# Kernel optimization log

Measured on AMD Instinct MI355X. Metric: run time of the kernel, lower is better.

Reference implementation:

```python
import jax, jax.numpy as jnp
import numpy as np

N_NODES = 100000
N_EDGES = 1600000
EDGES_IN = 1
HID = 64
OUT = 64


def setup_inputs() -> dict:
    key = jax.random.key(0)
    ks = jax.random.split(key, 10)
    s = lambda fan_in: 1.0 / np.sqrt(fan_in)
    inp = {
        "edge_index": jax.random.randint(ks[0], (2, N_EDGES), 0, N_NODES, dtype=jnp.int64) if jax.config.jax_enable_x64 else jax.random.randint(ks[0], (2, N_EDGES), 0, N_NODES, dtype=jnp.int32),
        "edge_attr": jax.random.normal(ks[1], (N_EDGES, EDGES_IN), dtype=jnp.float32),
        # edge MLP: Linear(EDGES_IN->HID), SiLU, Linear(HID->HID), SiLU
        "W1": jax.random.uniform(ks[2], (EDGES_IN, HID), jnp.float32, -s(EDGES_IN), s(EDGES_IN)),
        "b1": jax.random.uniform(ks[3], (HID,), jnp.float32, -s(EDGES_IN), s(EDGES_IN)),
        "W2": jax.random.uniform(ks[4], (HID, HID), jnp.float32, -s(HID), s(HID)),
        "b2": jax.random.uniform(ks[5], (HID,), jnp.float32, -s(HID), s(HID)),
        # node MLP: Linear(HID->HID), SiLU, Linear(HID->OUT)
        "W3": jax.random.uniform(ks[6], (HID, HID), jnp.float32, -s(HID), s(HID)),
        "b3": jax.random.uniform(ks[7], (HID,), jnp.float32, -s(HID), s(HID)),
        "W4": jax.random.uniform(ks[8], (HID, OUT), jnp.float32, -s(HID), s(HID)),
        "b4": jax.random.uniform(ks[9], (OUT,), jnp.float32, -s(HID), s(HID)),
    }
    return inp


def reference(edge_index, edge_attr, W1, b1, W2, b2, W3, b3, W4, b4):
    silu = jax.nn.silu
    # edge model: [E, EDGES_IN] -> [E, HID]
    ef = silu(edge_attr @ W1 + b1)
    ef = silu(ef @ W2 + b2)
    # unsorted_segment_sum over source nodes (row): [E, HID] -> [N, HID]
    row = edge_index[0]
    agg = jax.ops.segment_sum(ef, row, num_segments=N_NODES)
    # node model: [N, HID] -> [N, OUT]
    h = silu(agg @ W3 + b3) @ W4 + b4
    return h
```

## Files before the change

### kernel.cpp

```cpp
#include <hip/hip_runtime.h>
#include <math.h>
#include <utility>

#define TN 4096
#define XMIN (-8.0f)
#define XMAX (8.0f)

#define GB1 256
#define MAXBK 2048
#define BKN 64
#define BKCAP 1792

typedef __attribute__((ext_vector_type(8))) short short8;
typedef __attribute__((ext_vector_type(4))) float f32x4;

__device__ __forceinline__ float silu_f(float v) {
    return v / (1.0f + __expf(-v));
}

__device__ __forceinline__ unsigned short f2bf(float x) {
    unsigned u = __float_as_uint(x);
    return (unsigned short)((u + 0x7FFFu + ((u >> 16) & 1u)) >> 16);
}
__device__ __forceinline__ float bf2f(unsigned short h) {
    return __uint_as_float(((unsigned)h) << 16);
}

#define SPLIT8(w0,w1,w2,w3,w4,w5,w6,w7, H, L) { \
    unsigned short _h0=f2bf(w0),_h1=f2bf(w1),_h2=f2bf(w2),_h3=f2bf(w3), \
                   _h4=f2bf(w4),_h5=f2bf(w5),_h6=f2bf(w6),_h7=f2bf(w7); \
    H = (short8){(short)_h0,(short)_h1,(short)_h2,(short)_h3, \
                 (short)_h4,(short)_h5,(short)_h6,(short)_h7}; \
    L = (short8){(short)f2bf((w0)-bf2f(_h0)),(short)f2bf((w1)-bf2f(_h1)), \
                 (short)f2bf((w2)-bf2f(_h2)),(short)f2bf((w3)-bf2f(_h3)), \
                 (short)f2bf((w4)-bf2f(_h4)),(short)f2bf((w5)-bf2f(_h5)), \
                 (short)f2bf((w6)-bf2f(_h6)),(short)f2bf((w7)-bf2f(_h7))}; }

#define BFRAG(Wp, kc, nt, H, L) { \
    const float* _p = (Wp) + ((kc)*32 + quad*8)*64 + (nt)*16 + m; \
    SPLIT8(_p[0],_p[64],_p[128],_p[192],_p[256],_p[320],_p[384],_p[448], H, L) }

#define MFMA3(AH, AL, BH, BL, ACC) \
    ACC = __builtin_amdgcn_mfma_f32_16x16x32_bf16(AH, BH, ACC, 0, 0, 0); \
    ACC = __builtin_amdgcn_mfma_f32_16x16x32_bf16(AL, BH, ACC, 0, 0, 0); \
    ACC = __builtin_amdgcn_mfma_f32_16x16x32_bf16(AH, BL, ACC, 0, 0, 0);

__global__ void build_table_k(const float* __restrict__ W1, const float* __restrict__ b1,
                              const float* __restrict__ W2, const float* __restrict__ b2,
                              float* __restrict__ table2, int* __restrict__ cnt, int nbk) {
    int gid  = blockIdx.x * blockDim.x + threadIdx.x;
    if (gid < nbk) cnt[gid] = 0;
    int wave = gid >> 6;
    int lane = gid & 63;
    if (wave >= TN) return;
    const float step = (XMAX - XMIN) / (float)(TN - 1);
    float x  = XMIN + step * (float)wave;
    float h1 = silu_f(fmaf(x, W1[lane], b1[lane]));
    float acc = b2[lane];
#pragma unroll
    for (int k = 0; k < 64; ++k) {
        float h1k = __shfl(h1, k, 64);
        acc = fmaf(h1k, W2[k * 64 + lane], acc);
    }
    float val = silu_f(acc);
    table2[(size_t)wave * 128 + 2 * lane] = val;
    if (wave > 0)
        table2[(size_t)(wave - 1) * 128 + 2 * lane + 1] = val;
}

__global__ void pack_w_k(const float* __restrict__ W3, const float* __restrict__ W4,
                         short8* __restrict__ packW) {
    int t = threadIdx.x, lane = t & 63, wid = t >> 6;
    int m = lane & 15, quad = lane >> 4;
    for (int f = wid; f < 16; f += 4) {
        const float* Wp = (f < 8) ? W3 : W4;
        int kc = f & 1, nt = (f >> 1) & 3;
        short8 H, L;
        BFRAG(Wp, kc, nt, H, L)
        packW[(2 * f + 0) * 64 + lane] = H;
        packW[(2 * f + 1) * 64 + lane] = L;
    }
}

__global__ void bhist_k(const int* __restrict__ row, int* __restrict__ cnt,
                        int E, int nbk) {
    __shared__ int h[MAXBK];
    int t = threadIdx.x;
    for (int e = t; e < nbk; e += 256) h[e] = 0;
    __syncthreads();
    for (int i = blockIdx.x * 256 + t; i < E; i += 256 * GB1)
        atomicAdd(&h[row[i] >> 6], 1);
    __syncthreads();
    for (int e = t; e < nbk; e += 256)
        if (h[e]) atomicAdd(&cnt[e], h[e]);
}

__global__ void scan1_k(const int* __restrict__ cnt, int* __restrict__ bhs,
                        int* __restrict__ cur, int n) {
    __shared__ int b0[MAXBK], b1[MAXBK];
    int t = threadIdx.x;
    for (int e = t; e < MAXBK; e += 1024) b0[e] = (e < n) ? cnt[e] : 0;
    __syncthreads();
    int* src = b0; int* dst = b1;
    for (int d = 1; d < MAXBK; d <<= 1) {
        for (int e = t; e < MAXBK; e += 1024)
            dst[e] = src[e] + ((e >= d) ? src[e - d] : 0);
        __syncthreads();
        int* tmp = src; src = dst; dst = tmp;
    }
    for (int e = t; e < n; e += 1024) {
        int v = (e == 0) ? 0 : src[e - 1];
        bhs[e] = v; cur[e] = v;
    }
    if (t == 0) bhs[n] = src[n - 1];
}

__global__ void bscatter_k(const int* __restrict__ row, const float* __restrict__ x,
                           int* __restrict__ cur, unsigned int* __restrict__ packed,
                           int E, int nbk) {
    __shared__ int hist[MAXBK];
    int t = threadIdx.x;
    for (int e = t; e < nbk; e += 256) hist[e] = 0;
    __syncthreads();
    for (int i = blockIdx.x * 256 + t; i < E; i += 256 * GB1)
        atomicAdd(&hist[row[i] >> 6], 1);
    __syncthreads();
    int shift = (int)(((long)blockIdx.x * nbk) >> 8);
    for (int k = t; k < nbk; k += 256) {
        int e = k + shift; if (e >= nbk) e -= nbk;
        int c = hist[e];
        hist[e] = c ? atomicAdd(&cur[e], c) : 0;
    }
    __syncthreads();
    const float scale = (float)(TN - 1) / (XMAX - XMIN);
    for (int i = blockIdx.x * 256 + t; i < E; i += 256 * GB1) {
        int   r  = row[i];
        float xv = x[i];
        float tt = fminf(fmaxf((xv - XMIN) * scale, 0.f), (float)(TN - 1) - 0.001f);
        int   i0 = (int)tt;
        unsigned int q = min((unsigned int)((tt - (float)i0) * 8192.0f), 8191u);
        unsigned int pk = ((unsigned int)(r & 63) << 25) | ((unsigned int)i0 << 13) | q;
        int p = atomicAdd(&hist[r >> 6], 1);
        packed[p] = pk;
    }
}

__global__ __launch_bounds__(256, 8)
void gather_k(const unsigned int* __restrict__ packed, const int* __restrict__ bhs,
              const float* __restrict__ table2, float* __restrict__ aggOut, int N) {
    __shared__ unsigned int srt[BKCAP];
    __shared__ int hist[BKN + 1];
    __shared__ int curs[BKN];
    int t = threadIdx.x, lane = t & 63, wid = t >> 6;
    int b = blockIdx.x;

    int s   = bhs[b];
    int e_  = bhs[b + 1];
    int cnt = min(e_ - s, BKCAP);

    for (int i = t; i <= BKN; i += 256) hist[i] = 0;
    __syncthreads();
    for (int i = t; i < cnt; i += 256)
        atomicAdd(&hist[packed[s + i] >> 25], 1);
    __syncthreads();

    if (wid == 0) {
        int c = hist[lane];
        int sc = c;
#pragma unroll
        for (int d = 1; d < 64; d <<= 1) {
            int u = __shfl_up(sc, d, 64);
            if (lane >= d) sc += u;
        }
        hist[lane] = sc - c;  curs[lane] = sc - c;
        if (lane == 63) hist[BKN] = sc;
    }
    __syncthreads();

    for (int i = t; i < cnt; i += 256) {
        unsigned int p = packed[s + i];
        int pos = atomicAdd(&curs[p >> 25], 1);
        srt[pos] = p;
    }
    __syncthreads();

    const float2* tab = (const float2*)table2 + lane;
    for (int nl = wid; nl < BKN; nl += 4) {
        int n = (b << 6) + nl;
        if (n >= N) break;
        int beg = hist[nl], dn = hist[nl + 1] - beg;
        float a0 = 0.f, a1 = 0.f, a2 = 0.f, a3 = 0.f;
        int j = 0;
        for (; j + 4 <= dn; j += 4) {
            unsigned int p0 = srt[beg + j + 0];
            unsigned int p1 = srt[beg + j + 1];
            unsigned int p2 = srt[beg + j + 2];
            unsigned int p3 = srt[beg + j + 3];
            float2 uv0 = tab[(p0 >> 7) & 0x3FFC0u];
            float2 uv1 = tab[(p1 >> 7) & 0x3FFC0u];
            float2 uv2 = tab[(p2 >> 7) & 0x3FFC0u];
            float2 uv3 = tab[(p3 >> 7) & 0x3FFC0u];
            float f0 = (float)(p0 & 0x1FFFu) * (1.0f / 8192.0f);
            float f1 = (float)(p1 & 0x1FFFu) * (1.0f / 8192.0f);
            float f2 = (float)(p2 & 0x1FFFu) * (1.0f / 8192.0f);
            float f3 = (float)(p3 & 0x1FFFu) * (1.0f / 8192.0f);
            a0 = fmaf(f0, uv0.y - uv0.x, a0 + uv0.x);
            a1 = fmaf(f1, uv1.y - uv1.x, a1 + uv1.x);
            a2 = fmaf(f2, uv2.y - uv2.x, a2 + uv2.x);
            a3 = fmaf(f3, uv3.y - uv3.x, a3 + uv3.x);
        }
        for (; j < dn; ++j) {
            unsigned int p0 = srt[beg + j];
            float2 uv0 = tab[(p0 >> 7) & 0x3FFC0u];
            float f0 = (float)(p0 & 0x1FFFu) * (1.0f / 8192.0f);
            a0 = fmaf(f0, uv0.y - uv0.x, a0 + uv0.x);
        }
        aggOut[(size_t)n * 64 + lane] = (a0 + a1) + (a2 + a3);
    }
}

__global__ __launch_bounds__(256, 1)
void mlp_k(const short8* __restrict__ packW, const float* __restrict__ b3,
           const float* __restrict__ b4, float* __restrict__ h, int N) {
    __shared__ float gt[4][16 * 68];
    int t = threadIdx.x, lane = t & 63, wid = t >> 6;
    int m = lane & 15, quad = lane >> 4;
    long r0 = (long)blockIdx.x * 64 + wid * 16;
    if (r0 >= N) return;

    const short8* pw = packW + lane;
#define LDW(s) pw[(s) * 64]
    short8 B3h00=LDW( 0), B3l00=LDW( 1), B3h01=LDW( 2), B3l01=LDW( 3);
    short8 B3h10=LDW( 4), B3l10=LDW( 5), B3h11=LDW( 6), B3l11=LDW( 7);
    short8 B3h20=LDW( 8), B3l20=LDW( 9), B3h21=LDW(10), B3l21=LDW(11);
    short8 B3h30=LDW(12), B3l30=LDW(13), B3h31=LDW(14), B3l31=LDW(15);
    short8 B4h00=LDW(16), B4l00=LDW(17), B4h01=LDW(18), B4l01=LDW(19);
    short8 B4h10=LDW(20), B4l10=LDW(21), B4h11=LDW(22), B4l11=LDW(23);
    short8 B4h20=LDW(24), B4l20=LDW(25), B4h21=LDW(26), B4l21=LDW(27);
    short8 B4h30=LDW(28), B4l30=LDW(29), B4h31=LDW(30), B4l31=LDW(31);
#undef LDW

    long ra = r0 + m; if (ra > N - 1) ra = N - 1;
    const float* ap = h + ra * 64 + quad * 8;
    float4 p0 = *(const float4*)(ap);       float4 p1 = *(const float4*)(ap + 4);
    float4 p2 = *(const float4*)(ap + 32);  float4 p3 = *(const float4*)(ap + 36);
    short8 Ah0, Al0, Ah1, Al1;
    SPLIT8(p0.x,p0.y,p0.z,p0.w,p1.x,p1.y,p1.z,p1.w, Ah0, Al0)
    SPLIT8(p2.x,p2.y,p2.z,p2.w,p3.x,p3.y,p3.z,p3.w, Ah1, Al1)

    f32x4 acc0 = {0.f,0.f,0.f,0.f}, acc1 = {0.f,0.f,0.f,0.f};
    f32x4 acc2 = {0.f,0.f,0.f,0.f}, acc3 = {0.f,0.f,0.f,0.f};
    MFMA3(Ah0, Al0, B3h00, B3l00, acc0)  MFMA3(Ah1, Al1, B3h01, B3l01, acc0)
    MFMA3(Ah0, Al0, B3h10, B3l10, acc1)  MFMA3(Ah1, Al1, B3h11, B3l11, acc1)
    MFMA3(Ah0, Al0, B3h20, B3l20, acc2)  MFMA3(Ah1, Al1, B3h21, B3l21, acc2)
    MFMA3(Ah0, Al0, B3h30, B3l30, acc3)  MFMA3(Ah1, Al1, B3h31, B3l31, acc3)

    float* g = gt[wid];
    {
        float bv = b3[0*16 + m];
        g[(quad*4+0)*68 + 0*16 + m] = silu_f(acc0.x + bv);
        g[(quad*4+1)*68 + 0*16 + m] = silu_f(acc0.y + bv);
        g[(quad*4+2)*68 + 0*16 + m] = silu_f(acc0.z + bv);
        g[(quad*4+3)*68 + 0*16 + m] = silu_f(acc0.w + bv);
    }
    {
        float bv = b3[1*16 + m];
        g[(quad*4+0)*68 + 1*16 + m] = silu_f(acc1.x + bv);
        g[(quad*4+1)*68 + 1*16 + m] = silu_f(acc1.y + bv);
        g[(quad*4+2)*68 + 1*16 + m] = silu_f(acc1.z + bv);
        g[(quad*4+3)*68 + 1*16 + m] = silu_f(acc1.w + bv);
    }
    {
        float bv = b3[2*16 + m];
        g[(quad*4+0)*68 + 2*16 + m] = silu_f(acc2.x + bv);
        g[(quad*4+1)*68 + 2*16 + m] = silu_f(acc2.y + bv);
        g[(quad*4+2)*68 + 2*16 + m] = silu_f(acc2.z + bv);
        g[(quad*4+3)*68 + 2*16 + m] = silu_f(acc2.w + bv);
    }
    {
        float bv = b3[3*16 + m];
        g[(quad*4+0)*68 + 3*16 + m] = silu_f(acc3.x + bv);
        g[(quad*4+1)*68 + 3*16 + m] = silu_f(acc3.y + bv);
        g[(quad*4+2)*68 + 3*16 + m] = silu_f(acc3.z + bv);
        g[(quad*4+3)*68 + 3*16 + m] = silu_f(acc3.w + bv);
    }
    __syncthreads();

    const float* gp = g + m * 68 + quad * 8;
    float4 q0 = *(const float4*)(gp);       float4 q1 = *(const float4*)(gp + 4);
    float4 q2 = *(const float4*)(gp + 32);  float4 q3 = *(const float4*)(gp + 36);
    short8 Gh0, Gl0, Gh1, Gl1;
    SPLIT8(q0.x,q0.y,q0.z,q0.w,q1.x,q1.y,q1.z,q1.w, Gh0, Gl0)
    SPLIT8(q2.x,q2.y,q2.z,q2.w,q3.x,q3.y,q3.z,q3.w, Gh1, Gl1)

    f32x4 o0 = {0.f,0.f,0.f,0.f}, o1 = {0.f,0.f,0.f,0.f};
    f32x4 o2 = {0.f,0.f,0.f,0.f}, o3 = {0.f,0.f,0.f,0.f};
    MFMA3(Gh0, Gl0, B4h00, B4l00, o0)  MFMA3(Gh1, Gl1, B4h01, B4l01, o0)
    MFMA3(Gh0, Gl0, B4h10, B4l10, o1)  MFMA3(Gh1, Gl1, B4h11, B4l11, o1)
    MFMA3(Gh0, Gl0, B4h20, B4l20, o2)  MFMA3(Gh1, Gl1, B4h21, B4l21, o2)
    MFMA3(Gh0, Gl0, B4h30, B4l30, o3)  MFMA3(Gh1, Gl1, B4h31, B4l31, o3)

    long rw = r0 + quad * 4;
    float c0 = b4[0*16 + m], c1 = b4[1*16 + m], c2 = b4[2*16 + m], c3 = b4[3*16 + m];
    if (rw + 0 < N) { float* o = h + (rw+0)*64;
        o[ 0+m]=o0.x+c0; o[16+m]=o1.x+c1; o[32+m]=o2.x+c2; o[48+m]=o3.x+c3; }
    if (rw + 1 < N) { float* o = h + (rw+1)*64;
        o[ 0+m]=o0.y+c0; o[16+m]=o1.y+c1; o[32+m]=o2.y+c2; o[48+m]=o3.y+c3; }
    if (rw + 2 < N) { float* o = h + (rw+2)*64;
        o[ 0+m]=o0.z+c0; o[16+m]=o1.z+c1; o[32+m]=o2.z+c2; o[48+m]=o3.z+c3; }
    if (rw + 3 < N) { float* o = h + (rw+3)*64;
        o[ 0+m]=o0.w+c0; o[16+m]=o1.w+c1; o[32+m]=o2.w+c2; o[48+m]=o3.w+c3; }
}

__global__ void zero_k(float4* __restrict__ p, int n4) {
    int i = blockIdx.x * blockDim.x + threadIdx.x;
    int stride = gridDim.x * blockDim.x;
    float4 z = make_float4(0.f, 0.f, 0.f, 0.f);
    for (; i < n4; i += stride) p[i] = z;
}

__global__ void edge_k(const int* __restrict__ row, const float* __restrict__ xarr,
                       const float* __restrict__ table2, float* __restrict__ agg, int E) {
    int gid    = blockIdx.x * blockDim.x + threadIdx.x;
    int lane   = gid & 63;
    int wave   = gid >> 6;
    int nwaves = (gridDim.x * blockDim.x) >> 6;
    const float scale = (float)(TN - 1) / (XMAX - XMIN);
    const float2* tab = (const float2*)table2 + lane;
    for (int e = wave; e < E; e += nwaves) {
        float x = xarr[e];
        int   r = row[e];
        float t = fminf(fmaxf((x - XMIN) * scale, 0.0f), (float)(TN - 1) - 0.001f);
        int   i0 = (int)t;
        float f  = t - (float)i0;
        float2 uv = tab[i0 << 6];
        atomicAdd(agg + (size_t)r * 64 + lane, fmaf(f, uv.y - uv.x, uv.x));
    }
}

extern "C" void kernel_launch(void* const* d_in, const int* in_sizes, int n_in,
                              void* d_out, int out_size, void* d_ws, size_t ws_size,
                              hipStream_t stream) {
    const int*   edge_index = (const int*)  d_in[0];
    const float* edge_attr  = (const float*)d_in[1];
    const float* W1 = (const float*)d_in[2];
    const float* b1 = (const float*)d_in[3];
    const float* W2 = (const float*)d_in[4];
    const float* b2 = (const float*)d_in[5];
    const float* W3 = (const float*)d_in[6];
    const float* b3 = (const float*)d_in[7];
    const float* W4 = (const float*)d_in[8];
    const float* b4 = (const float*)d_in[9];

    float* out = (float*)d_out;
    const int E   = in_sizes[1];
    const int N   = out_size / 64;
    const int nbk = (N + 63) >> 6;
    const int nmb = (N + 63) / 64;

    char* ws = (char*)d_ws;
    size_t off = 0;
    auto carve = [&](size_t bytes) { size_t r = off; off = (off + bytes + 255) & ~(size_t)255; return r; };
    size_t tableOff = carve((size_t)TN * 128 * 4);
    size_t packWOff = carve((size_t)32 * 64 * 16);
    size_t cntOff   = carve((size_t)nbk * 4);
    size_t bhsOff   = carve((size_t)(nbk + 1) * 4);
    size_t curOff   = carve((size_t)nbk * 4);
    size_t pkOff    = carve((size_t)E * 4);
    bool fits = (off <= ws_size) && (nbk <= MAXBK);

    float*  table2 = (float*)(ws + tableOff);
    short8* packW  = (short8*)(ws + packWOff);
    int*    cnt    = (int*)(ws + cntOff);

    build_table_k<<<TN / 4, 256, 0, stream>>>(W1, b1, W2, b2, table2, cnt,
                                              fits ? nbk : 0);
    pack_w_k<<<1, 256, 0, stream>>>(W3, W4, packW);

    if (fits) {
        int* bhs = (int*)(ws + bhsOff);
        int* cur = (int*)(ws + curOff);
        unsigned int* packed = (unsigned int*)(ws + pkOff);

        bhist_k   <<<GB1, 256, 0, stream>>>(edge_index, cnt, E, nbk);
        scan1_k   <<<1, 1024, 0, stream>>>(cnt, bhs, cur, nbk);
        bscatter_k<<<GB1, 256, 0, stream>>>(edge_index, edge_attr, cur, packed, E, nbk);
        gather_k  <<<nbk, 256, 0, stream>>>(packed, bhs, table2, out, N);
        mlp_k     <<<nmb, 256, 0, stream>>>(packW, b3, b4, out, N);
    } else {
        zero_k<<<4096, 256, 0, stream>>>((float4*)out, (N * 64) / 4);
        edge_k<<<8192, 256, 0, stream>>>(edge_index, edge_attr, table2, out, E);
        mlp_k <<<nmb, 256, 0, stream>>>(packW, b3, b4, out, N);
    }
}
```

Baseline: 210.8 us.

## Replace bucketed counting sort with padded per-node slots plus overflow list

After: 302.6 us. 43.5% more time.

```diff
diff --git a/kernel.cpp b/kernel.cpp
--- a/kernel.cpp
+++ b/kernel.cpp
@@ -6,10 +6,7 @@
 #define XMIN (-8.0f)
 #define XMAX (8.0f)
 
-#define GB1 256
-#define MAXBK 2048
-#define BKN 64
-#define BKCAP 1792
+#define OVFCAP 32768
 
 typedef __attribute__((ext_vector_type(8))) short short8;
 typedef __attribute__((ext_vector_type(4))) float f32x4;
@@ -47,9 +44,9 @@
 
 __global__ void build_table_k(const float* __restrict__ W1, const float* __restrict__ b1,
                               const float* __restrict__ W2, const float* __restrict__ b2,
-                              float* __restrict__ table2, int* __restrict__ cnt, int nbk) {
+                              float* __restrict__ table2, int* __restrict__ cnt, int ncnt) {
     int gid  = blockIdx.x * blockDim.x + threadIdx.x;
-    if (gid < nbk) cnt[gid] = 0;
+    if (gid < ncnt) cnt[gid] = 0;
     int wave = gid >> 6;
     int lane = gid & 63;
     if (wave >= TN) return;
@@ -82,140 +79,86 @@
     }
 }
 
-__global__ void bhist_k(const int* __restrict__ row, int* __restrict__ cnt,
-                        int E, int nbk) {
-    __shared__ int h[MAXBK];
-    int t = threadIdx.x;
-    for (int e = t; e < nbk; e += 256) h[e] = 0;
-    __syncthreads();
-    for (int i = blockIdx.x * 256 + t; i < E; i += 256 * GB1)
-        atomicAdd(&h[row[i] >> 6], 1);
-    __syncthreads();
-    for (int e = t; e < nbk; e += 256)
-        if (h[e]) atomicAdd(&cnt[e], h[e]);
-}
-
-__global__ void scan1_k(const int* __restrict__ cnt, int* __restrict__ bhs,
-                        int* __restrict__ cur, int n) {
-    __shared__ int b0[MAXBK], b1[MAXBK];
-    int t = threadIdx.x;
-    for (int e = t; e < MAXBK; e += 1024) b0[e] = (e < n) ? cnt[e] : 0;
-    __syncthreads();
-    int* src = b0; int* dst = b1;
-    for (int d = 1; d < MAXBK; d <<= 1) {
-        for (int e = t; e < MAXBK; e += 1024)
-            dst[e] = src[e] + ((e >= d) ? src[e - d] : 0);
-        __syncthreads();
-        int* tmp = src; src = dst; dst = tmp;
-    }
-    for (int e = t; e < n; e += 1024) {
-        int v = (e == 0) ? 0 : src[e - 1];
-        bhs[e] = v; cur[e] = v;
-    }
-    if (t == 0) bhs[n] = src[n - 1];
-}
-
-__global__ void bscatter_k(const int* __restrict__ row, const float* __restrict__ x,
-                           int* __restrict__ cur, unsigned int* __restrict__ packed,
-                           int E, int nbk) {
-    __shared__ int hist[MAXBK];
-    int t = threadIdx.x;
-    for (int e = t; e < nbk; e += 256) hist[e] = 0;
-    __syncthreads();
-    for (int i = blockIdx.x * 256 + t; i < E; i += 256 * GB1)
-        atomicAdd(&hist[row[i] >> 6], 1);
-    __syncthreads();
-    int shift = (int)(((long)blockIdx.x * nbk) >> 8);
-    for (int k = t; k < nbk; k += 256) {
-        int e = k + shift; if (e >= nbk) e -= nbk;
-        int c = hist[e];
-        hist[e] = c ? atomicAdd(&cur[e], c) : 0;
-    }
-    __syncthreads();
+__global__ void scatter_k(const int* __restrict__ row, const float* __restrict__ x,
+                          int* __restrict__ cnt, unsigned int* __restrict__ padded,
+                          unsigned int* __restrict__ ovf, int E, int pad, int N) {
+    int i = blockIdx.x * 256 + threadIdx.x;
+    int stride = gridDim.x * 256;
     const float scale = (float)(TN - 1) / (XMAX - XMIN);
-    for (int i = blockIdx.x * 256 + t; i < E; i += 256 * GB1) {
+    for (; i < E; i += stride) {
         int   r  = row[i];
         float xv = x[i];
         float tt = fminf(fmaxf((xv - XMIN) * scale, 0.f), (float)(TN - 1) - 0.001f);
         int   i0 = (int)tt;
-        unsigned int q = min((unsigned int)((tt - (float)i0) * 8192.0f), 8191u);
-        unsigned int pk = ((unsigned int)(r & 63) << 25) | ((unsigned int)i0 << 13) | q;
-        int p = atomicAdd(&hist[r >> 6], 1);
-        packed[p] = pk;
+        unsigned int q  = min((unsigned int)((tt - (float)i0) * 8192.0f), 8191u);
+        unsigned int pk = ((unsigned int)i0 << 13) | q;
+        int pos = atomicAdd(&cnt[r], 1);
+        if (pos < pad) {
+            padded[(size_t)r * pad + pos] = pk;
+        } else {
+            int o = atomicAdd(&cnt[N], 1);
+            if (o < OVFCAP) { ovf[2 * o] = (unsigned int)r; ovf[2 * o + 1] = pk; }
+        }
     }
 }
 
 __global__ __launch_bounds__(256, 8)
-void gather_k(const unsigned int* __restrict__ packed, const int* __restrict__ bhs,
-              const float* __restrict__ table2, float* __restrict__ aggOut, int N) {
-    __shared__ unsigned int srt[BKCAP];
-    __shared__ int hist[BKN + 1];
-    __shared__ int curs[BKN];
+void gather_k(const unsigned int* __restrict__ padded, const int* __restrict__ cnt,
+              const float* __restrict__ table2, float* __restrict__ aggOut,
+              int N, int pad) {
     int t = threadIdx.x, lane = t & 63, wid = t >> 6;
-    int b = blockIdx.x;
-
-    int s   = bhs[b];
-    int e_  = bhs[b + 1];
-    int cnt = min(e_ - s, BKCAP);
-
-    for (int i = t; i <= BKN; i += 256) hist[i] = 0;
-    __syncthreads();
-    for (int i = t; i < cnt; i += 256)
-        atomicAdd(&hist[packed[s + i] >> 25], 1);
-    __syncthreads();
-
-    if (wid == 0) {
-        int c = hist[lane];
-        int sc = c;
-#pragma unroll
-        for (int d = 1; d < 64; d <<= 1) {
-            int u = __shfl_up(sc, d, 64);
-            if (lane >= d) sc += u;
-        }
-        hist[lane] = sc - c;  curs[lane] = sc - c;
-        if (lane == 63) hist[BKN] = sc;
-    }
-    __syncthreads();
-
-    for (int i = t; i < cnt; i += 256) {
-        unsigned int p = packed[s + i];
-        int pos = atomicAdd(&curs[p >> 25], 1);
-        srt[pos] = p;
-    }
-    __syncthreads();
+    int n = blockIdx.x * 4 + wid;
+    if (n >= N) return;
+    int dn = min(cnt[n], pad);
+
+    size_t idx = (size_t)n * pad + lane;
+    size_t last = (size_t)N * pad - 1;
+    unsigned int w = padded[idx <= last ? idx : last];
 
     const float2* tab = (const float2*)table2 + lane;
-    for (int nl = wid; nl < BKN; nl += 4) {
-        int n = (b << 6) + nl;
-        if (n >= N) break;
-        int beg = hist[nl], dn = hist[nl + 1] - beg;
-        float a0 = 0.f, a1 = 0.f, a2 = 0.f, a3 = 0.f;
-        int j = 0;
-        for (; j + 4 <= dn; j += 4) {
-            unsigned int p0 = srt[beg + j + 0];
-            unsigned int p1 = srt[beg + j + 1];
-            unsigned int p2 = srt[beg + j + 2];
-            unsigned int p3 = srt[beg + j + 3];
-            float2 uv0 = tab[(p0 >> 7) & 0x3FFC0u];
-            float2 uv1 = tab[(p1 >> 7) & 0x3FFC0u];
-            float2 uv2 = tab[(p2 >> 7) & 0x3FFC0u];
-            float2 uv3 = tab[(p3 >> 7) & 0x3FFC0u];
-            float f0 = (float)(p0 & 0x1FFFu) * (1.0f / 8192.0f);
-            float f1 = (float)(p1 & 0x1FFFu) * (1.0f / 8192.0f);
-            float f2 = (float)(p2 & 0x1FFFu) * (1.0f / 8192.0f);
-            float f3 = (float)(p3 & 0x1FFFu) * (1.0f / 8192.0f);
-            a0 = fmaf(f0, uv0.y - uv0.x, a0 + uv0.x);
-            a1 = fmaf(f1, uv1.y - uv1.x, a1 + uv1.x);
-            a2 = fmaf(f2, uv2.y - uv2.x, a2 + uv2.x);
-            a3 = fmaf(f3, uv3.y - uv3.x, a3 + uv3.x);
-        }
-        for (; j < dn; ++j) {
-            unsigned int p0 = srt[beg + j];
-            float2 uv0 = tab[(p0 >> 7) & 0x3FFC0u];
-            float f0 = (float)(p0 & 0x1FFFu) * (1.0f / 8192.0f);
-            a0 = fmaf(f0, uv0.y - uv0.x, a0 + uv0.x);
-        }
-        aggOut[(size_t)n * 64 + lane] = (a0 + a1) + (a2 + a3);
+    float a0 = 0.f, a1 = 0.f, a2 = 0.f, a3 = 0.f;
+    int j = 0;
+    for (; j + 4 <= dn; j += 4) {
+        unsigned int p0 = __shfl(w, j + 0, 64);
+        unsigned int p1 = __shfl(w, j + 1, 64);
+        unsigned int p2 = __shfl(w, j + 2, 64);
+        unsigned int p3 = __shfl(w, j + 3, 64);
+        float2 uv0 = tab[(size_t)(p0 >> 13) << 6];
+        float2 uv1 = tab[(size_t)(p1 >> 13) << 6];
+        float2 uv2 = tab[(size_t)(p2 >> 13) << 6];
+        float2 uv3 = tab[(size_t)(p3 >> 13) << 6];
+        float f0 = (float)(p0 & 0x1FFFu) * (1.0f / 8192.0f);
+        float f1 = (float)(p1 & 0x1FFFu) * (1.0f / 8192.0f);
+        float f2 = (float)(p2 & 0x1FFFu) * (1.0f / 8192.0f);
+        float f3 = (float)(p3 & 0x1FFFu) * (1.0f / 8192.0f);
+        a0 = fmaf(f0, uv0.y - uv0.x, a0 + uv0.x);
+        a1 = fmaf(f1, uv1.y - uv1.x, a1 + uv1.x);
+        a2 = fmaf(f2, uv2.y - uv2.x, a2 + uv2.x);
+        a3 = fmaf(f3, uv3.y - uv3.x, a3 + uv3.x);
+    }
+    for (; j < dn; ++j) {
+        unsigned int p0 = __shfl(w, j, 64);
+        float2 uv0 = tab[(size_t)(p0 >> 13) << 6];
+        float f0 = (float)(p0 & 0x1FFFu) * (1.0f / 8192.0f);
+        a0 = fmaf(f0, uv0.y - uv0.x, a0 + uv0.x);
+    }
+    aggOut[(size_t)n * 64 + lane] = (a0 + a1) + (a2 + a3);
+}
+
+__global__ void ovf_k(const unsigned int* __restrict__ ovf, const int* __restrict__ cnt,
+                      const float* __restrict__ table2, float* __restrict__ agg, int N) {
+    int m = min(cnt[N], OVFCAP);
+    if (m == 0) return;
+    int lane = threadIdx.x & 63;
+    int wv   = (blockIdx.x * 256 + threadIdx.x) >> 6;
+    int nwv  = (gridDim.x * 256) >> 6;
+    const float2* tab = (const float2*)table2 + lane;
+    for (int e = wv; e < m; e += nwv) {
+        unsigned int r  = ovf[2 * e];
+        unsigned int pk = ovf[2 * e + 1];
+        float2 uv = tab[(size_t)(pk >> 13) << 6];
+        float f = (float)(pk & 0x1FFFu) * (1.0f / 8192.0f);
+        atomicAdd(agg + (size_t)r * 64 + lane, fmaf(f, uv.y - uv.x, uv.x));
     }
 }
 
@@ -355,7 +298,6 @@
     float* out = (float*)d_out;
     const int E   = in_sizes[1];
     const int N   = out_size / 64;
-    const int nbk = (N + 63) >> 6;
     const int nmb = (N + 63) / 64;
 
     char* ws = (char*)d_ws;
@@ -363,30 +305,34 @@
     auto carve = [&](size_t bytes) { size_t r = off; off = (off + bytes + 255) & ~(size_t)255; return r; };
     size_t tableOff = carve((size_t)TN * 128 * 4);
     size_t packWOff = carve((size_t)32 * 64 * 16);
-    size_t cntOff   = carve((size_t)nbk * 4);
-    size_t bhsOff   = carve((size_t)(nbk + 1) * 4);
-    size_t curOff   = carve((size_t)nbk * 4);
-    size_t pkOff    = carve((size_t)E * 4);
-    bool fits = (off <= ws_size) && (nbk <= MAXBK);
+    size_t cntOff   = carve((size_t)(N + 1) * 4);
+    size_t ovfOff   = carve((size_t)OVFCAP * 8);
+
+    int pad = 0;
+    size_t padOff = off;
+    if (off < ws_size) {
+        size_t slots = (ws_size - off) / ((size_t)N * 4);
+        pad = (int)(slots > 64 ? 64 : slots) & ~15;
+    }
+    bool fits = (pad >= 32);
 
     float*  table2 = (float*)(ws + tableOff);
     short8* packW  = (short8*)(ws + packWOff);
     int*    cnt    = (int*)(ws + cntOff);
 
     build_table_k<<<TN / 4, 256, 0, stream>>>(W1, b1, W2, b2, table2, cnt,
-                                              fits ? nbk : 0);
+                                              fits ? (N + 1) : 0);
     pack_w_k<<<1, 256, 0, stream>>>(W3, W4, packW);
 
     if (fits) {
-        int* bhs = (int*)(ws + bhsOff);
-        int* cur = (int*)(ws + curOff);
-        unsigned int* packed = (unsigned int*)(ws + pkOff);
-
-        bhist_k   <<<GB1, 256, 0, stream>>>(edge_index, cnt, E, nbk);
-        scan1_k   <<<1, 1024, 0, stream>>>(cnt, bhs, cur, nbk);
-        bscatter_k<<<GB1, 256, 0, stream>>>(edge_index, edge_attr, cur, packed, E, nbk);
-        gather_k  <<<nbk, 256, 0, stream>>>(packed, bhs, table2, out, N);
-        mlp_k     <<<nmb, 256, 0, stream>>>(packW, b3, b4, out, N);
+        unsigned int* padded = (unsigned int*)(ws + padOff);
+        unsigned int* ovf    = (unsigned int*)(ws + ovfOff);
+
+        scatter_k<<<2048, 256, 0, stream>>>(edge_index, edge_attr, cnt, padded,
+                                            ovf, E, pad, N);
+        gather_k <<<(N + 3) / 4, 256, 0, stream>>>(padded, cnt, table2, out, N, pad);
+        ovf_k    <<<8, 256, 0, stream>>>(ovf, cnt, table2, out, N);
+        mlp_k    <<<nmb, 256, 0, stream>>>(packW, b3, b4, out, N);
     } else {
         zero_k<<<4096, 256, 0, stream>>>((float4*)out, (N * 64) / 4);
         edge_k<<<8192, 256, 0, stream>>>(edge_index, edge_attr, table2, out, E);
```
